# Optimization experiments

Measured on AMD Instinct MI355X. Metric: run time of the kernel, lower is better.

## Reference

```python
import jax, jax.numpy as jnp
import numpy as np

D_MODEL = 1024
NUM_HEADS = 16
D_K = D_MODEL // NUM_HEADS
TEMPERATURE = 1.0
EPS = 1e-6


def setup_inputs() -> dict:
    key = jax.random.key(0)
    ks = jax.random.split(key, 8)
    B, S, D, H = 2, 2048, D_MODEL, NUM_HEADS
    sc = 1.0 / np.sqrt(D)
    x = jax.random.normal(ks[0], (B, S, D), dtype=jnp.float32)
    Wq = jax.random.normal(ks[1], (D, D), dtype=jnp.float32) * sc
    Wk = jax.random.normal(ks[2], (D, D), dtype=jnp.float32) * sc
    Wv = jax.random.normal(ks[3], (D, D), dtype=jnp.float32) * sc
    Wo = jax.random.normal(ks[4], (D, D), dtype=jnp.float32) * sc
    bo = jnp.zeros((D,), dtype=jnp.float32)
    phase_scale = jnp.ones((H,), dtype=jnp.float32)
    # orthogonal init for entanglement matrix
    q, _ = np.linalg.qr(np.random.default_rng(0).normal(size=(H, H)))
    ent = jnp.asarray(q, dtype=jnp.float32)
    gamma = jnp.ones((D,), dtype=jnp.float32)
    beta = jnp.zeros((D,), dtype=jnp.float32)
    return {"x": x, "Wq": Wq, "Wk": Wk, "Wv": Wv, "Wo": Wo, "bo": bo,
            "phase_scale": phase_scale, "ent": ent, "gamma": gamma, "beta": beta}


def reference(x, Wq, Wk, Wv, Wo, bo, phase_scale, ent, gamma, beta):
    B, S, D = x.shape
    H, dk = NUM_HEADS, D_K
    # projections -> [B, H, S, dk]
    Q = (x @ Wq).reshape(B, S, H, dk).transpose(0, 2, 1, 3)
    K = (x @ Wk).reshape(B, S, H, dk).transpose(0, 2, 1, 3)
    V = (x @ Wv).reshape(B, S, H, dk).transpose(0, 2, 1, 3)
    # per-head QK^T, scaled, phase-modulated
    scores = jnp.einsum('bhqd,bhkd->bhqk', Q, K)
    inv = 1.0 / (float(np.sqrt(dk)) * TEMPERATURE)
    s = scores * (inv * phase_scale)[None, :, None, None]
    # real part of quantum phase: cos(s) + 0.1*cos(2s)  (imag part of V is zero,
    # so head_output = attended_real; the 0.1*attended_imag term vanishes)
    w = jnp.cos(s) + 0.1 * jnp.cos(2.0 * s)
    w = jax.nn.softmax(w, axis=-1)
    att = jnp.einsum('bhqk,bhkd->bhqd', w, V).transpose(0, 2, 1, 3)  # [B,S,H,dk]
    # faithful reproduction of tf.einsum('bsnd,hm->bsmd', ...): sums over n AND h
    att = jnp.einsum('bsnd,hm->bsmd', att, ent)
    out = att.reshape(B, S, D) @ Wo + bo
    r = out + x
    mu = jnp.mean(r, axis=-1, keepdims=True)
    var = jnp.mean(jnp.square(r - mu), axis=-1, keepdims=True)
    return gamma * (r - mu) * jax.lax.rsqrt(var + EPS) + beta
```

## Files before the change

### kernel.cpp

```cpp
#include <hip/hip_runtime.h>
#include <cstdint>
#include <cstddef>

#define S_LEN 2048
#define DMODEL 1024
#define NHEADS 16
#define DKH 64
#define MROWS 4096
#define BH_CNT 32

typedef __bf16 bf16x8 __attribute__((ext_vector_type(8)));
typedef __bf16 bf16x2 __attribute__((ext_vector_type(2)));
typedef float f32x4 __attribute__((ext_vector_type(4)));
typedef unsigned int u32x4 __attribute__((ext_vector_type(4)));
typedef unsigned int u32;
typedef unsigned short u16;

__device__ __forceinline__ u16 f2bfu(float f) {
  u32 u = __float_as_uint(f);
  return (u16)((u + 0x7FFFu + ((u >> 16) & 1u)) >> 16);
}

__device__ __forceinline__ float bf2f(u16 v) {
  return __uint_as_float((u32)v << 16);
}

__device__ __forceinline__ u32 pk_bf16(float a, float b) {
  bf16x2 v;
  v[0] = (__bf16)a;
  v[1] = (__bf16)b;
  return __builtin_bit_cast(u32, v);
}

__device__ __forceinline__ void pl32swap(u32& a, u32& b) {
#if __has_builtin(__builtin_amdgcn_permlane32_swap)
  auto r = __builtin_amdgcn_permlane32_swap((int)a, (int)b, false, false);
  a = (u32)r[0]; b = (u32)r[1];
#else
  asm volatile("v_permlane32_swap_b32 %0, %1" : "+v"(a), "+v"(b));
#endif
}
__device__ __forceinline__ void pl16swap(u32& a, u32& b) {
#if __has_builtin(__builtin_amdgcn_permlane16_swap)
  auto r = __builtin_amdgcn_permlane16_swap((int)a, (int)b, false, false);
  a = (u32)r[0]; b = (u32)r[1];
#else
  asm volatile("v_permlane16_swap_b32 %0, %1" : "+v"(a), "+v"(b));
#endif
}

__device__ __forceinline__ void gload16(void* lds, const void* g) {
  __builtin_amdgcn_global_load_lds(
      (const __attribute__((address_space(1))) void*)g,
      (__attribute__((address_space(3))) void*)lds, 16, 0, 0);
}

__global__ __launch_bounds__(256) void prep_all_k(const float* __restrict__ x,
    const float* __restrict__ Wq, const float* __restrict__ Wk,
    const float* __restrict__ Wv, const float* __restrict__ Wo,
    const float* __restrict__ ps, const float* __restrict__ ent,
    u16* __restrict__ xb, u16* __restrict__ Wb, float* __restrict__ Woeff) {
  __shared__ float tile[32][33];
  int bid = blockIdx.x;
  int t = threadIdx.x;
  if (bid < 4096) {
    int i = (bid * 256 + t) * 4;
    float4 v = *(const float4*)(x + i);
    *(uint2*)(xb + i) = make_uint2(pk_bf16(v.x, v.y), pk_bf16(v.z, v.w));
  } else if (bid < 7168) {
    int lb = bid - 4096;
    int sel = lb >> 10, rem = lb & 1023;
    int k0 = (rem & 31) * 32, c0 = (rem >> 5) * 32;
    const float* W = sel == 0 ? Wq : (sel == 1 ? Wk : Wv);
    int tx = t & 31, ty = t >> 5;
#pragma unroll
    for (int i = 0; i < 4; ++i)
      tile[ty + i * 8][tx] = W[(size_t)(k0 + ty + i * 8) * DMODEL + c0 + tx];
    __syncthreads();
#pragma unroll
    for (int i = 0; i < 4; ++i) {
      int row = ty + i * 8;
      float v = tile[tx][row];
      if (sel == 1) v *= 0.019894367886486918f * ps[(c0 + row) >> 6];
      Wb[(size_t)(sel * 1024 + c0 + row) * DMODEL + k0 + tx] = f2bfu(v);
    }
  } else {
    __shared__ float e[16];
    if (t < 16) {
      float s = 0.f;
#pragma unroll
      for (int h = 0; h < 16; ++h) s += ent[h * 16 + t];
      e[t] = s;
    }
    __syncthreads();
    int gid = (bid - 7168) * 256 + t;
    int d = gid >> 10, j = gid & 1023;
    float acc = 0.f;
#pragma unroll
    for (int m = 0; m < 16; ++m) acc += e[m] * Wo[(size_t)((m << 6) + d) * DMODEL + j];
    Woeff[(size_t)d * DMODEL + j] = acc;
  }
}

__global__ __launch_bounds__(512, 2) void gemm_qkv_k(const u16* __restrict__ xb,
    const u16* __restrict__ Wb, u16* __restrict__ Qb, u16* __restrict__ Kb,
    u16* __restrict__ Vt) {
  __shared__ __align__(16) u16 As[2][8192];
  __shared__ __align__(16) u16 Bs[2][8192];
  int bid = blockIdx.x;
  int xcd = bid & 7, wi = bid >> 3;
  int mt = (xcd >> 1) * 4 + (wi & 3);
  int nt = (xcd & 1) * 6 + (wi >> 2);
  int m0 = mt * 256, n0 = nt * 256;
  int tid = threadIdx.x;
  int lane = tid & 63, w = tid >> 6;
  int c = lane & 15, g = lane >> 4;
  int wr = w >> 2, wcn = w & 3;

  int r2 = tid >> 2, s2 = tid & 3;
  const u16* aS = xb + (size_t)(m0 + r2) * DMODEL + ((s2 ^ (r2 & 3)) * 8);
  const u16* bS = Wb + (size_t)(n0 + r2) * DMODEL + ((s2 ^ (r2 & 3)) * 8);

  int xorc = (g ^ (c & 3)) * 8;
  int aoff[8], boff[4];
#pragma unroll
  for (int mf = 0; mf < 8; ++mf) aoff[mf] = (wr * 128 + mf * 16 + c) * 32 + xorc;
#pragma unroll
  for (int nf = 0; nf < 4; ++nf) boff[nf] = (wcn * 64 + nf * 16 + c) * 32 + xorc;

  f32x4 acc[8][4];
#pragma unroll
  for (int i = 0; i < 8; ++i)
#pragma unroll
    for (int j = 0; j < 4; ++j) acc[i][j] = (f32x4){0.f, 0.f, 0.f, 0.f};

  auto stage = [&](int buf, int kt) {
    gload16(&As[buf][tid * 8], aS + kt);
    gload16(&As[buf][4096 + tid * 8], aS + 128 * DMODEL + kt);
    gload16(&Bs[buf][tid * 8], bS + kt);
    gload16(&Bs[buf][4096 + tid * 8], bS + 128 * DMODEL + kt);
  };
  auto compute = [&](const int off) {
    bf16x8 bfr[4];
#pragma unroll
    for (int nf = 0; nf < 4; ++nf) bfr[nf] = *(const bf16x8*)(&Bs[0][0] + off + boff[nf]);
#pragma unroll
    for (int mf = 0; mf < 8; ++mf) {
      bf16x8 af = *(const bf16x8*)(&As[0][0] + off + aoff[mf]);
#pragma unroll
      for (int nf = 0; nf < 4; ++nf)
        acc[mf][nf] = __builtin_amdgcn_mfma_f32_16x16x32_bf16(af, bfr[nf], acc[mf][nf], 0, 0, 0);
    }
  };

  stage(0, 0);
  __syncthreads();
  for (int kt = 0; kt < DMODEL; kt += 64) {
    stage(1, kt + 32);
    compute(0);
    __syncthreads();
    if (kt + 64 < DMODEL) stage(0, kt + 64);
    compute(8192);
    __syncthreads();
  }

  int sel = nt >> 2;
  int h0 = (nt & 3) * 4;
  int b = m0 >> 11, sbase = m0 & 2047;
  char* Ls = (char*)&As[0][0];
#pragma unroll
  for (int half = 0; half < 2; ++half) {
    if (wr == half) {
      if (sel == 2) {
#pragma unroll
        for (int mf = 0; mf < 8; ++mf)
#pragma unroll
          for (int nf = 0; nf < 4; ++nf) {
            int n = wcn * 64 + nf * 16 + c;
            int mh = mf * 16 + 4 * g;
            *(uint2*)(Ls + n * 256 + ((mh * 2) ^ ((n & 7) << 4))) =
                make_uint2(pk_bf16(acc[mf][nf][0], acc[mf][nf][1]),
                           pk_bf16(acc[mf][nf][2], acc[mf][nf][3]));
          }
      } else {
#pragma unroll
        for (int mf = 0; mf < 8; ++mf)
#pragma unroll
          for (int nf = 0; nf < 4; ++nf) {
            int n = wcn * 64 + nf * 16 + c;
#pragma unroll
            for (int j = 0; j < 4; ++j) {
              int mh = mf * 16 + 4 * g + j;
              __bf16 hv = (__bf16)acc[mf][nf][j];
              *(u16*)(Ls + mh * 512 + ((n * 2) ^ ((mh & 7) << 4))) =
                  __builtin_bit_cast(u16, hv);
            }
          }
      }
    }
    __syncthreads();
    if (sel == 2) {
      int n = tid >> 1, cc = tid & 1;
      int head = h0 + (n >> 6), d = n & 63;
      u16* dst = Vt + ((size_t)(b * 16 + head) * DKH + d) * S_LEN + sbase + half * 128 + cc * 64;
#pragma unroll
      for (int kk = 0; kk < 8; ++kk)
        *(uint4*)(dst + kk * 8) =
            *(const uint4*)(Ls + n * 256 + ((cc * 128 + kk * 16) ^ ((n & 7) << 4)));
    } else {
      int r = tid >> 2, cc = tid & 3;
      int head = h0 + cc;
      u16* base = (sel == 0 ? Qb : Kb);
      u16* dst = base + ((size_t)(b * 16 + head) * S_LEN + sbase + half * 128 + r) * DKH;
#pragma unroll
      for (int kk = 0; kk < 8; ++kk)
        *(uint4*)(dst + kk * 8) =
            *(const uint4*)(Ls + r * 512 + ((cc * 128 + kk * 16) ^ ((r & 7) << 4)));
    }
    __syncthreads();
  }
}

__global__ __launch_bounds__(512) void attn_k(const u16* __restrict__ Qb,
    const u16* __restrict__ Kb, const u16* __restrict__ Vt,
    u16* __restrict__ attbufb) {
  __shared__ __align__(16) u16 Ks[4][4096];
  __shared__ __align__(16) u16 Vs[4][4096];
  __shared__ float dred[8][2][16];
  int fid = blockIdx.x;
  int swz = (fid & 7) * 64 + (fid >> 3);
  int bh = swz >> 4, qb = swz & 15;
  int tid = threadIdx.x;
  int lane = tid & 63, w = tid >> 6;
  int c = lane & 15, g = lane >> 4;
  int grp = w >> 2, h = (w >> 1) & 1, qh = w & 1;
  int q0 = qb * 128 + grp * 64;
  const float L2E = 1.4426950408889634f;

  const u16* Kbase = Kb + (size_t)bh * S_LEN * DKH;
  const u16* Vbase = Vt + (size_t)bh * DKH * S_LEN;

  int srow = w * 8 + (lane >> 3), slot = lane & 7, kp = slot ^ (srow & 7);
  const u16* kSrc = Kbase + (size_t)srow * DKH + kp * 8;
  const u16* vSrc = Vbase + (size_t)srow * S_LEN + kp * 8;
  auto stage = [&](int buf, int tile) {
    gload16(&Ks[buf][w * 512], kSrc + (size_t)tile * 64 * DKH);
    gload16(&Vs[buf][w * 512], vSrc + tile * 64);
  };

  int rot = qb * 2;
  stage(0, rot & 31);
  stage(1, (rot + 1) & 31);

  bf16x8 qf[2][2];
#pragma unroll
  for (int qg = 0; qg < 2; ++qg) {
    const u16* qp = Qb + ((size_t)bh * S_LEN + q0 + qh * 32 + qg * 16 + c) * DKH + g * 8;
    qf[qg][0] = *(const bf16x8*)qp;
    qf[qg][1] = *(const bf16x8*)(qp + 32);
  }
  bf16x8 onesf;
#pragma unroll
  for (int i = 0; i < 8; ++i) onesf[i] = (__bf16)1.0f;

  const u16* kptr[2][2];
#pragma unroll
  for (int fm = 0; fm < 2; ++fm) {
    int row = h * 32 + fm * 16 + c;
    kptr[fm][0] = &Ks[0][row * 64 + ((g ^ (row & 7)) * 8)];
    kptr[fm][1] = &Ks[0][row * 64 + (((4 + g) ^ (row & 7)) * 8)];
  }
  const u16* vptr[4];
#pragma unroll
  for (int fd = 0; fd < 4; ++fd) {
    int vrow = fd * 16 + c;
    vptr[fd] = &Vs[0][vrow * 64 + (((4 * h + g) ^ (vrow & 7)) * 8)];
  }

  f32x4 attT[4][2];
#pragma unroll
  for (int i = 0; i < 4; ++i)
#pragma unroll
    for (int qg = 0; qg < 2; ++qg) attT[i][qg] = (f32x4){0.f, 0.f, 0.f, 0.f};
  f32x4 denacc[2];
  denacc[0] = (f32x4){0.f, 0.f, 0.f, 0.f};
  denacc[1] = (f32x4){0.f, 0.f, 0.f, 0.f};

  auto qk = [&](const int off, f32x4 (&sT)[2][2]) {
    __builtin_amdgcn_s_setprio(1);
#pragma unroll
    for (int fm = 0; fm < 2; ++fm) {
      bf16x8 a0 = *(const bf16x8*)(kptr[fm][0] + off);
      bf16x8 a1 = *(const bf16x8*)(kptr[fm][1] + off);
#pragma unroll
      for (int qg = 0; qg < 2; ++qg) {
        f32x4 z = (f32x4){0.f, 0.f, 0.f, 0.f};
        z = __builtin_amdgcn_mfma_f32_16x16x32_bf16(a0, qf[qg][0], z, 0, 0, 0);
        sT[fm][qg] = __builtin_amdgcn_mfma_f32_16x16x32_bf16(a1, qf[qg][1], z, 0, 0, 0);
      }
    }
    __builtin_amdgcn_s_setprio(0);
  };
  auto smpv = [&](f32x4 (&sT)[2][2], const int off) {
    u32 wq[2][2][2];
#pragma unroll
    for (int fm = 0; fm < 2; ++fm)
#pragma unroll
      for (int qg = 0; qg < 2; ++qg) {
        float pv[4];
#pragma unroll
        for (int j = 0; j < 4; ++j) {
          float cv = __builtin_amdgcn_cosf(sT[fm][qg][j]);
          float w2 = __fmaf_rn(cv, __fmaf_rn(0.2f * L2E, cv, L2E), -0.1f * L2E);
          pv[j] = __builtin_amdgcn_exp2f(w2);
        }
        wq[qg][fm][0] = pk_bf16(pv[0], pv[1]);
        wq[qg][fm][1] = pk_bf16(pv[2], pv[3]);
      }
    bf16x8 pf[2];
#pragma unroll
    for (int qg = 0; qg < 2; ++qg) {
      u32 b0 = wq[qg][0][0], b2 = wq[qg][1][0];
      pl32swap(b0, b2);
      pl16swap(b0, b2);
      u32 b1 = wq[qg][0][1], b3 = wq[qg][1][1];
      pl32swap(b1, b3);
      pl16swap(b1, b3);
      pf[qg] = __builtin_bit_cast(bf16x8, (u32x4){b0, b1, b2, b3});
    }
    __builtin_amdgcn_s_setprio(1);
#pragma unroll
    for (int fd = 0; fd < 4; ++fd) {
      bf16x8 vf = *(const bf16x8*)(vptr[fd] + off);
#pragma unroll
      for (int qg = 0; qg < 2; ++qg)
        attT[fd][qg] = __builtin_amdgcn_mfma_f32_16x16x32_bf16(vf, pf[qg], attT[fd][qg], 0, 0, 0);
    }
#pragma unroll
    for (int qg = 0; qg < 2; ++qg)
      denacc[qg] = __builtin_amdgcn_mfma_f32_16x16x32_bf16(onesf, pf[qg], denacc[qg], 0, 0, 0);
    __builtin_amdgcn_s_setprio(0);
  };

  f32x4 sA[2][2], sB[2][2];
  __syncthreads();
  for (int t = 0; t < 32; t += 4) {
    stage(2, (t + 2 + rot) & 31);
    stage(3, (t + 3 + rot) & 31);
    qk(0, sA);
    qk(4096, sB);
    smpv(sA, 0);
    smpv(sB, 4096);
    __syncthreads();
    if (t + 4 < 32) {
      stage(0, (t + 4 + rot) & 31);
      stage(1, (t + 5 + rot) & 31);
    }
    qk(8192, sA);
    qk(12288, sB);
    smpv(sA, 8192);
    smpv(sB, 12288);
    __syncthreads();
  }

  if (g == 0) {
    dred[w][0][c] = denacc[0][0];
    dred[w][1][c] = denacc[1][0];
  }
  float* Rq = (grp ? (float*)&Vs[0][0] : (float*)&Ks[0][0]) + qh * 2048;
  if (h == 1) {
#pragma unroll
    for (int fd = 0; fd < 4; ++fd)
#pragma unroll
      for (int qg = 0; qg < 2; ++qg)
        *(f32x4*)&Rq[(qg * 16 + c) * 64 + fd * 16 + 4 * g] = attT[fd][qg];
  }
  __syncthreads();
  if (h == 0) {
    float inv[2];
#pragma unroll
    for (int qg = 0; qg < 2; ++qg)
      inv[qg] = 1.f / (dred[w][qg][c] + dred[w ^ 2][qg][c]);
#pragma unroll
    for (int fd = 0; fd < 4; ++fd)
#pragma unroll
      for (int qg = 0; qg < 2; ++qg) {
        f32x4 part = *(const f32x4*)&Rq[(qg * 16 + c) * 64 + fd * 16 + 4 * g];
        f32x4 tot = (attT[fd][qg] + part) * inv[qg];
        int q = q0 + qh * 32 + qg * 16 + c;
        *(uint2*)(attbufb + ((size_t)bh * S_LEN + q) * DKH + fd * 16 + 4 * g) =
            make_uint2(pk_bf16(tot[0], tot[1]), pk_bf16(tot[2], tot[3]));
      }
  }
}

__global__ __launch_bounds__(256) void fuse_out_ln_k(const u16* __restrict__ attbufb,
    const float* __restrict__ Woeff, const float* __restrict__ bo,
    const float* __restrict__ x, const float* __restrict__ gamma,
    const float* __restrict__ beta, float* __restrict__ out) {
  __shared__ float red[8][256];
  __shared__ __align__(16) float a[8][64];
  __shared__ float sred[8][4][2];
  int t = threadIdx.x;
  int r0 = blockIdx.x * 8;
  int d = t & 63, hg = t >> 6;
#pragma unroll
  for (int rr = 0; rr < 8; ++rr) {
    int m = r0 + rr, b = m >> 11, sr = m & 2047;
    float pa = 0.f;
#pragma unroll
    for (int hh = 0; hh < 4; ++hh) {
      int h = hg * 4 + hh;
      pa += bf2f(attbufb[(((size_t)(b * 16 + h)) * S_LEN + sr) * DKH + d]);
    }
    red[rr][t] = pa;
  }
  __syncthreads();
#pragma unroll
  for (int e = 0; e < 2; ++e) {
    int idx = t + e * 256;
    int rr = idx >> 6, dd = idx & 63;
    a[rr][dd] = red[rr][dd] + red[rr][64 + dd] + red[rr][128 + dd] + red[rr][192 + dd];
  }
  __syncthreads();

  float o[8][4];
#pragma unroll
  for (int rr = 0; rr < 8; ++rr) { o[rr][0] = o[rr][1] = o[rr][2] = o[rr][3] = 0.f; }
  int c4 = t * 4;
  for (int dd = 0; dd < 64; dd += 4) {
    float4 wv0 = *(const float4*)(Woeff + (size_t)(dd + 0) * DMODEL + c4);
    float4 wv1 = *(const float4*)(Woeff + (size_t)(dd + 1) * DMODEL + c4);
    float4 wv2 = *(const float4*)(Woeff + (size_t)(dd + 2) * DMODEL + c4);
    float4 wv3 = *(const float4*)(Woeff + (size_t)(dd + 3) * DMODEL + c4);
#pragma unroll
    for (int rr = 0; rr < 8; ++rr) {
      float4 av = *(const float4*)&a[rr][dd];
      o[rr][0] += av.x * wv0.x + av.y * wv1.x + av.z * wv2.x + av.w * wv3.x;
      o[rr][1] += av.x * wv0.y + av.y * wv1.y + av.z * wv2.y + av.w * wv3.y;
      o[rr][2] += av.x * wv0.z + av.y * wv1.z + av.z * wv2.z + av.w * wv3.z;
      o[rr][3] += av.x * wv0.w + av.y * wv1.w + av.z * wv2.w + av.w * wv3.w;
    }
  }
  float4 bv = *(const float4*)(bo + c4);
  int w = t >> 6, lane = t & 63;
#pragma unroll
  for (int rr = 0; rr < 8; ++rr) {
    int m = r0 + rr;
    float4 xv = *(const float4*)(x + (size_t)m * DMODEL + c4);
    o[rr][0] += bv.x + xv.x;
    o[rr][1] += bv.y + xv.y;
    o[rr][2] += bv.z + xv.z;
    o[rr][3] += bv.w + xv.w;
    float s = o[rr][0] + o[rr][1] + o[rr][2] + o[rr][3];
    float q = o[rr][0] * o[rr][0] + o[rr][1] * o[rr][1] + o[rr][2] * o[rr][2] + o[rr][3] * o[rr][3];
#pragma unroll
    for (int mm = 1; mm < 64; mm <<= 1) {
      s += __shfl_xor(s, mm, 64);
      q += __shfl_xor(q, mm, 64);
    }
    if (lane == 0) { sred[rr][w][0] = s; sred[rr][w][1] = q; }
  }
  __syncthreads();
  float4 gv = *(const float4*)(gamma + c4);
  float4 bev = *(const float4*)(beta + c4);
#pragma unroll
  for (int rr = 0; rr < 8; ++rr) {
    float s = sred[rr][0][0] + sred[rr][1][0] + sred[rr][2][0] + sred[rr][3][0];
    float q = sred[rr][0][1] + sred[rr][1][1] + sred[rr][2][1] + sred[rr][3][1];
    float mu = s * (1.f / 1024.f);
    float var = q * (1.f / 1024.f) - mu * mu;
    float rs = rsqrtf(var + 1e-6f);
    int m = r0 + rr;
    float4 ov;
    ov.x = gv.x * (o[rr][0] - mu) * rs + bev.x;
    ov.y = gv.y * (o[rr][1] - mu) * rs + bev.y;
    ov.z = gv.z * (o[rr][2] - mu) * rs + bev.z;
    ov.w = gv.w * (o[rr][3] - mu) * rs + bev.w;
    *(float4*)(out + (size_t)m * DMODEL + c4) = ov;
  }
}

extern "C" void kernel_launch(void* const* d_in, const int* in_sizes, int n_in,
                              void* d_out, int out_size, void* d_ws, size_t ws_size,
                              hipStream_t stream) {
  const float* x = (const float*)d_in[0];
  const float* Wq = (const float*)d_in[1];
  const float* Wk = (const float*)d_in[2];
  const float* Wv = (const float*)d_in[3];
  const float* Wo = (const float*)d_in[4];
  const float* bo = (const float*)d_in[5];
  const float* ps = (const float*)d_in[6];
  const float* ent = (const float*)d_in[7];
  const float* gamma = (const float*)d_in[8];
  const float* beta = (const float*)d_in[9];
  float* out = (float*)d_out;

  char* ws = (char*)d_ws;
  size_t o = 0;
  u16* xb = (u16*)(ws + o);    o += (size_t)MROWS * DMODEL * 2;
  u16* Wb = (u16*)(ws + o);    o += (size_t)3072 * 1024 * 2;
  u16* Qb = (u16*)(ws + o);    o += (size_t)BH_CNT * S_LEN * DKH * 2;
  u16* Kb = (u16*)(ws + o);    o += (size_t)BH_CNT * S_LEN * DKH * 2;
  u16* Vt = (u16*)(ws + o);    o += (size_t)BH_CNT * S_LEN * DKH * 2;
  float* Woeff = (float*)(ws + o);   o += (size_t)DKH * DMODEL * 4;
  u16* attbufb = (u16*)(ws + o);     o += (size_t)BH_CNT * S_LEN * DKH * 2;

  prep_all_k<<<dim3(7424), dim3(256), 0, stream>>>(x, Wq, Wk, Wv, Wo, ps, ent,
                                                   xb, Wb, Woeff);
  gemm_qkv_k<<<dim3(192), dim3(512), 0, stream>>>(xb, Wb, Qb, Kb, Vt);
  attn_k<<<dim3(512), dim3(512), 0, stream>>>(Qb, Kb, Vt, attbufb);
  fuse_out_ln_k<<<dim3(512), dim3(256), 0, stream>>>(attbufb, Woeff, bo, x, gamma, beta, out);
}
```

Measured before the change: 124.2 us.

## Restructure QKV GEMM main loop into 8-phase ping-pong pipeline with 64-wide K tiles

Rewrites the QKV projection GEMM main loop to use 64-wide K tiles in a single 128 KB LDS buffer (double-buffered), with loads split into quarter-stages interleaved between four MFMA sub-blocks, explicit s_barrier/vmcnt waits and setprio around MFMA clusters. The aim is to overlap global->LDS traffic with compute and cut barrier frequency per K element. It drops occupancy to one block per CU (launch bounds 512,1) and relies on hand-tuned wait counts, risking hazards if the vmcnt accounting is off.

```diff
diff --git a/kernel.cpp b/kernel.cpp
--- a/kernel.cpp
+++ b/kernel.cpp
@@ -54,6 +54,14 @@
       (const __attribute__((address_space(1))) void*)g,
       (__attribute__((address_space(3))) void*)lds, 16, 0, 0);
 }
+
+#define WAITV(n)                                            \
+  do {                                                      \
+    asm volatile("s_waitcnt vmcnt(" #n ")" ::: "memory");   \
+    __builtin_amdgcn_sched_barrier(0);                      \
+  } while (0)
+
+#define SBAR() asm volatile("s_barrier" ::: "memory")
 
 __global__ __launch_bounds__(256) void prep_all_k(const float* __restrict__ x,
     const float* __restrict__ Wq, const float* __restrict__ Wk,
@@ -102,11 +110,10 @@
   }
 }
 
-__global__ __launch_bounds__(512, 2) void gemm_qkv_k(const u16* __restrict__ xb,
+__global__ __launch_bounds__(512, 1) void gemm_qkv_k(const u16* __restrict__ xb,
     const u16* __restrict__ Wb, u16* __restrict__ Qb, u16* __restrict__ Kb,
     u16* __restrict__ Vt) {
-  __shared__ __align__(16) u16 As[2][8192];
-  __shared__ __align__(16) u16 Bs[2][8192];
+  __shared__ __align__(16) u16 SM[65536];
   int bid = blockIdx.x;
   int xcd = bid & 7, wi = bid >> 3;
   int mt = (xcd >> 1) * 4 + (wi & 3);
@@ -117,16 +124,25 @@
   int c = lane & 15, g = lane >> 4;
   int wr = w >> 2, wcn = w & 3;
 
-  int r2 = tid >> 2, s2 = tid & 3;
-  const u16* aS = xb + (size_t)(m0 + r2) * DMODEL + ((s2 ^ (r2 & 3)) * 8);
-  const u16* bS = Wb + (size_t)(n0 + r2) * DMODEL + ((s2 ^ (r2 & 3)) * 8);
-
-  int xorc = (g ^ (c & 3)) * 8;
-  int aoff[8], boff[4];
-#pragma unroll
-  for (int mf = 0; mf < 8; ++mf) aoff[mf] = (wr * 128 + mf * 16 + c) * 32 + xorc;
-#pragma unroll
-  for (int nf = 0; nf < 4; ++nf) boff[nf] = (wcn * 64 + nf * 16 + c) * 32 + xorc;
+  int srow8 = tid >> 3;
+  int sch = (tid & 7) ^ (srow8 & 7);
+  const u16* aS = xb + (size_t)(m0 + srow8) * DMODEL + sch * 8;
+  const u16* bS = Wb + (size_t)(n0 + srow8) * DMODEL + sch * 8;
+
+  int cho[2];
+  cho[0] = (g ^ (c & 7)) * 8;
+  cho[1] = ((4 + g) ^ (c & 7)) * 8;
+  const u16* aRow = SM + wr * 8192 + c * 64;
+  const u16* bRow = SM + 16384 + (wcn >> 1) * 8192 + ((wcn & 1) * 64 + c) * 64;
+
+  auto stA = [&](int d, int h, int kt) {
+    gload16(SM + d + h * 8192 + tid * 8, aS + (size_t)(h * 128) * DMODEL + kt);
+    gload16(SM + d + h * 8192 + 4096 + tid * 8, aS + (size_t)(h * 128 + 64) * DMODEL + kt);
+  };
+  auto stB = [&](int d, int h, int kt) {
+    gload16(SM + d + 16384 + h * 8192 + tid * 8, bS + (size_t)(h * 128) * DMODEL + kt);
+    gload16(SM + d + 16384 + h * 8192 + 4096 + tid * 8, bS + (size_t)(h * 128 + 64) * DMODEL + kt);
+  };
 
   f32x4 acc[8][4];
 #pragma unroll
@@ -134,40 +150,109 @@
 #pragma unroll
     for (int j = 0; j < 4; ++j) acc[i][j] = (f32x4){0.f, 0.f, 0.f, 0.f};
 
-  auto stage = [&](int buf, int kt) {
-    gload16(&As[buf][tid * 8], aS + kt);
-    gload16(&As[buf][4096 + tid * 8], aS + 128 * DMODEL + kt);
-    gload16(&Bs[buf][tid * 8], bS + kt);
-    gload16(&Bs[buf][4096 + tid * 8], bS + 128 * DMODEL + kt);
-  };
-  auto compute = [&](const int off) {
-    bf16x8 bfr[4];
-#pragma unroll
-    for (int nf = 0; nf < 4; ++nf) bfr[nf] = *(const bf16x8*)(&Bs[0][0] + off + boff[nf]);
-#pragma unroll
-    for (int mf = 0; mf < 8; ++mf) {
-      bf16x8 af = *(const bf16x8*)(&As[0][0] + off + aoff[mf]);
-#pragma unroll
-      for (int nf = 0; nf < 4; ++nf)
-        acc[mf][nf] = __builtin_amdgcn_mfma_f32_16x16x32_bf16(af, bfr[nf], acc[mf][nf], 0, 0, 0);
-    }
-  };
-
-  stage(0, 0);
-  __syncthreads();
-  for (int kt = 0; kt < DMODEL; kt += 64) {
-    stage(1, kt + 32);
-    compute(0);
-    __syncthreads();
-    if (kt + 64 < DMODEL) stage(0, kt + 64);
-    compute(8192);
-    __syncthreads();
-  }
-
+  bf16x8 a03[4][2], a47[4][2], b01[2][2], b23[2][2];
+
+  auto rdA03 = [&](const int d) {
+#pragma unroll
+    for (int mf = 0; mf < 4; ++mf)
+#pragma unroll
+      for (int kk = 0; kk < 2; ++kk)
+        a03[mf][kk] = *(const bf16x8*)(aRow + d + mf * 1024 + cho[kk]);
+  };
+  auto rdA47 = [&](const int d) {
+#pragma unroll
+    for (int mf = 0; mf < 4; ++mf)
+#pragma unroll
+      for (int kk = 0; kk < 2; ++kk)
+        a47[mf][kk] = *(const bf16x8*)(aRow + d + (4 + mf) * 1024 + cho[kk]);
+  };
+  auto rdB01 = [&](const int d) {
+#pragma unroll
+    for (int nf = 0; nf < 2; ++nf)
+#pragma unroll
+      for (int kk = 0; kk < 2; ++kk)
+        b01[nf][kk] = *(const bf16x8*)(bRow + d + nf * 1024 + cho[kk]);
+  };
+  auto rdB23 = [&](const int d) {
+#pragma unroll
+    for (int nf = 0; nf < 2; ++nf)
+#pragma unroll
+      for (int kk = 0; kk < 2; ++kk)
+        b23[nf][kk] = *(const bf16x8*)(bRow + d + (2 + nf) * 1024 + cho[kk]);
+  };
+  auto mm = [&](bf16x8 (&aa)[4][2], bf16x8 (&bb)[2][2], const int mb, const int nb) {
+    __builtin_amdgcn_s_setprio(1);
+#pragma unroll
+    for (int mf = 0; mf < 4; ++mf)
+#pragma unroll
+      for (int nf = 0; nf < 2; ++nf)
+#pragma unroll
+        for (int kk = 0; kk < 2; ++kk)
+          acc[mb + mf][nb + nf] =
+              __builtin_amdgcn_mfma_f32_16x16x32_bf16(aa[mf][kk], bb[nf][kk], acc[mb + mf][nb + nf], 0, 0, 0);
+    __builtin_amdgcn_s_setprio(0);
+  };
+
+  stA(0, 0, 0); stA(0, 1, 0); stB(0, 0, 0); stB(0, 1, 0);
+  stA(32768, 0, 64); stA(32768, 1, 64);
+  __syncthreads();
+
+  for (int j = 0; j < 8; ++j) {
+    const bool more = (j < 7);
+    int kt1 = (2 * j + 1) * 64, kt2 = (2 * j + 2) * 64, kt3 = (2 * j + 3) * 64;
+    rdA03(0); rdB01(0);
+    stB(32768, 0, kt1);
+    SBAR();
+    mm(a03, b01, 0, 0);
+    SBAR();
+    rdA47(0);
+    stB(32768, 1, kt1);
+    SBAR();
+    mm(a47, b01, 4, 0);
+    SBAR();
+    rdB23(0);
+    if (more) stA(0, 0, kt2);
+    SBAR();
+    mm(a03, b23, 0, 2);
+    SBAR();
+    if (more) {
+      stA(0, 1, kt2);
+      WAITV(4);
+    } else {
+      WAITV(0);
+    }
+    SBAR();
+    mm(a47, b23, 4, 2);
+    SBAR();
+    rdA03(32768); rdB01(32768);
+    if (more) stB(0, 0, kt2);
+    SBAR();
+    mm(a03, b01, 0, 0);
+    SBAR();
+    rdA47(32768);
+    if (more) stB(0, 1, kt2);
+    SBAR();
+    mm(a47, b01, 4, 0);
+    SBAR();
+    rdB23(32768);
+    if (more) stA(32768, 0, kt3);
+    SBAR();
+    mm(a03, b23, 0, 2);
+    SBAR();
+    if (more) {
+      stA(32768, 1, kt3);
+      WAITV(4);
+    }
+    SBAR();
+    mm(a47, b23, 4, 2);
+    SBAR();
+  }
+
+  __syncthreads();
   int sel = nt >> 2;
   int h0 = (nt & 3) * 4;
   int b = m0 >> 11, sbase = m0 & 2047;
-  char* Ls = (char*)&As[0][0];
+  char* Ls = (char*)&SM[0];
 #pragma unroll
   for (int half = 0; half < 2; ++half) {
     if (wr == half) {
@@ -189,9 +274,9 @@
           for (int nf = 0; nf < 4; ++nf) {
             int n = wcn * 64 + nf * 16 + c;
 #pragma unroll
-            for (int j = 0; j < 4; ++j) {
-              int mh = mf * 16 + 4 * g + j;
-              __bf16 hv = (__bf16)acc[mf][nf][j];
+            for (int jj = 0; jj < 4; ++jj) {
+              int mh = mf * 16 + 4 * g + jj;
+              __bf16 hv = (__bf16)acc[mf][nf][jj];
               *(u16*)(Ls + mh * 512 + ((n * 2) ^ ((mh & 7) << 4))) =
                   __builtin_bit_cast(u16, hv);
             }
```

Measured after the change: 121.1 us. -2.5%, faster.
